# Optimization experiments

Measured on AMD Instinct MI355X. Metric: run time of the kernel, lower is better.

## Reference

```python
import jax, jax.numpy as jnp
import numpy as np

N = 50000
E = 1600000
IN_CH = 128
HID = 32
HEADS = 4
OUT_CH = 64
NEG_SLOPE = 0.2


def _seg_softmax(e, seg, n):
    # e: [E,H], seg: [E] destination indices -> per-destination softmax
    m = jax.ops.segment_max(e, seg, num_segments=n)          # [N,H]
    ex = jnp.exp(e - m[seg])
    s = jax.ops.segment_sum(ex, seg, num_segments=n)         # [N,H]
    return ex / (s[seg] + 1e-16)


def _gat_conv(x, edge_index, W, a_src, a_dst, b, concat):
    # x: [N,Fin]; W: [Fin, H*C]; a_src/a_dst: [H,C]; b: [H*C] or [C]
    H, C = a_src.shape
    n = x.shape[0]
    h = (x @ W).reshape(n, H, C)                              # [N,H,C]
    src, dst = edge_index[0], edge_index[1]
    as_ = jnp.einsum('nhc,hc->nh', h, a_src)                  # [N,H]
    ad_ = jnp.einsum('nhc,hc->nh', h, a_dst)
    e = jax.nn.leaky_relu(as_[src] + ad_[dst], NEG_SLOPE)     # [E,H]
    alpha = _seg_softmax(e, dst, n)                           # [E,H]
    msg = h[src] * alpha[:, :, None]                          # [E,H,C]
    out = jax.ops.segment_sum(msg, dst, num_segments=n)       # [N,H,C]
    out = out.reshape(n, H * C) if concat else out.mean(axis=1)
    return out + b, alpha


def _layer_norm(x, w, b, eps=1e-5):
    mu = x.mean(-1, keepdims=True)
    var = x.var(-1, keepdims=True)
    return (x - mu) * jax.lax.rsqrt(var + eps) * w + b


def setup_inputs() -> dict:
    key = jax.random.key(0)
    ks = jax.random.split(key, 20)
    g = lambda k, s: jax.random.normal(k, s, dtype=jnp.float32) * 0.05
    d = {
        'x': jax.random.normal(ks[0], (N, IN_CH), dtype=jnp.float32),
        'edge_index': jax.random.randint(ks[1], (2, E), 0, N, dtype=jnp.int64),
        # gat1: in=IN_CH, out=HID, heads, concat
        'W1': g(ks[2], (IN_CH, HEADS * HID)),
        'a_src1': g(ks[3], (HEADS, HID)),
        'a_dst1': g(ks[4], (HEADS, HID)),
        'b1': jnp.zeros((HEADS * HID,), jnp.float32),
        'ln1_w': jnp.ones((HEADS * HID,), jnp.float32),
        'ln1_b': jnp.zeros((HEADS * HID,), jnp.float32),
        'Wskip': g(ks[5], (IN_CH, HEADS * HID)),
        'bskip': jnp.zeros((HEADS * HID,), jnp.float32),
        # gat2: in=HEADS*HID, out=HID, concat
        'W2': g(ks[6], (HEADS * HID, HEADS * HID)),
        'a_src2': g(ks[7], (HEADS, HID)),
        'a_dst2': g(ks[8], (HEADS, HID)),
        'b2': jnp.zeros((HEADS * HID,), jnp.float32),
        'ln2_w': jnp.ones((HEADS * HID,), jnp.float32),
        'ln2_b': jnp.zeros((HEADS * HID,), jnp.float32),
        # gat3: in=HEADS*HID, out=OUT_CH, concat=False (mean over heads)
        'W3': g(ks[9], (HEADS * HID, HEADS * OUT_CH)),
        'a_src3': g(ks[10], (HEADS, OUT_CH)),
        'a_dst3': g(ks[11], (HEADS, OUT_CH)),
        'b3': jnp.zeros((OUT_CH,), jnp.float32),
    }
    return d


def reference(x, edge_index, W1, a_src1, a_dst1, b1, ln1_w, ln1_b,
              Wskip, bskip, W2, a_src2, a_dst2, b2, ln2_w, ln2_b,
              W3, a_src3, a_dst3, b3):
    x_skip = x
    h, alpha1 = _gat_conv(x, edge_index, W1, a_src1, a_dst1, b1, concat=True)
    h = jax.nn.elu(h)
    h = _layer_norm(h, ln1_w, ln1_b)
    h = h + (x_skip @ Wskip + bskip)
    h, alpha2 = _gat_conv(h, edge_index, W2, a_src2, a_dst2, b2, concat=True)
    h = jax.nn.elu(h)
    h = _layer_norm(h, ln2_w, ln2_b)
    out, alpha3 = _gat_conv(h, edge_index, W3, a_src3, a_dst3, b3, concat=False)
    return out, alpha1, alpha2, alpha3
```

## Files before the change

kernel.cpp:

```cpp
#include <hip/hip_runtime.h>

#define NN 50000
#define EE 1600000
#define SCAN_B 196
#define NB 196
#define CHUNK 2048
#define G1 782
#define L1 (NB * G1)
#define B1 599

typedef __attribute__((ext_vector_type(8))) short bf16x8;
typedef __attribute__((ext_vector_type(4))) float f32x4;
typedef __attribute__((ext_vector_type(2))) float f32x2;

#if __has_builtin(__builtin_elementwise_fma)
#define PKFMA(a, b, c) __builtin_elementwise_fma((a), (b), (c))
#else
#define PKFMA(a, b, c) ((a) * (b) + (c))
#endif

__device__ __forceinline__ float bfu(unsigned short u) { return __uint_as_float((unsigned)u << 16); }
__device__ __forceinline__ float bflo(unsigned u) { return __uint_as_float(u << 16); }
__device__ __forceinline__ float bfhi(unsigned u) { return __uint_as_float(u & 0xffff0000u); }
__device__ __forceinline__ f32x2 bfpk(unsigned u) {
    f32x2 r; r.x = bflo(u); r.y = bfhi(u); return r;
}
__device__ __forceinline__ unsigned short f2bf(float f) {
    unsigned u = __float_as_uint(f);
    u += 0x7fff + ((u >> 16) & 1);
    return (unsigned short)(u >> 16);
}
__device__ __forceinline__ unsigned pk2(float a, float b) {
    return (unsigned)f2bf(a) | ((unsigned)f2bf(b) << 16);
}
__device__ __forceinline__ float cvt_load(const void* p, int i, bool f32) {
    if (f32) return ((const float*)p)[i];
    return bfu(((const unsigned short*)p)[i]);
}

__global__ void detect_k(const void* ei_raw, const void* x_raw, int* flags) {
    __shared__ int s_i64, s_f32;
    const int t = threadIdx.x;
    if (t == 0) { s_i64 = 1; s_f32 = 0; }
    __syncthreads();
    const int* ei32 = (const int*)ei_raw;
    if (ei32[2 * t + 1] != 0) atomicAnd(&s_i64, 0);
    const unsigned short* xu = (const unsigned short*)x_raw;
    int found = 0;
    for (int j = 0; j < 32; j++) {
        unsigned short u = xu[t * 32 + j];
        if ((u & 0x7F80) == 0x7F80) found = 1;
    }
    if (found) atomicOr(&s_f32, 1);
    __syncthreads();
    if (t == 0) { flags[0] = s_i64; flags[1] = s_f32; }
}

__global__ __launch_bounds__(256) void hist1_k(const void* ei_raw, const int* flags,
                                               int2* __restrict__ edges, int* __restrict__ cnt)
{
    __shared__ int h[NB];
    const int t = threadIdx.x;
    const int i64 = __builtin_amdgcn_readfirstlane(flags[0]);
    if (t < NB) h[t] = 0;
    __syncthreads();
    const int beg = blockIdx.x * CHUNK;
    const int end = min(beg + CHUNK, EE);
    for (int e = beg + t; e < end; e += 256) {
        int2 v;
        if (i64) { const long long* p = (const long long*)ei_raw; v.x = (int)p[e]; v.y = (int)p[EE + e]; }
        else     { const int* p = (const int*)ei_raw;             v.x = p[e];      v.y = p[EE + e];      }
        edges[e] = v;
        atomicAdd(&h[v.y >> 8], 1);
    }
    __syncthreads();
    if (t < NB) cnt[(size_t)t * G1 + blockIdx.x] = h[t];
}

__global__ __launch_bounds__(256) void scanAg_k(int* __restrict__ cnt, int* __restrict__ bsum2) {
    __shared__ int ps[256];
    const int b = blockIdx.x, t = threadIdx.x;
    const int i = b * 256 + t;
    const int v = (i < L1) ? cnt[i] : 0;
    ps[t] = v;
    __syncthreads();
    for (int off = 1; off < 256; off <<= 1) {
        const int u = (t >= off) ? ps[t - off] : 0;
        __syncthreads();
        ps[t] += u;
        __syncthreads();
    }
    if (i < L1) cnt[i] = ps[t] - v;
    if (t == 255) bsum2[b] = ps[255];
}
__global__ void scanBg_k(int* bsum2) {
    __shared__ int ps[256];
    const int t = threadIdx.x;
    int vals[3];
    int s = 0;
    #pragma unroll
    for (int i = 0; i < 3; i++) {
        const int idx = t * 3 + i;
        vals[i] = (idx < B1) ? bsum2[idx] : 0;
        s += vals[i];
    }
    ps[t] = s;
    __syncthreads();
    for (int off = 1; off < 256; off <<= 1) {
        const int u = (t >= off) ? ps[t - off] : 0;
        __syncthreads();
        ps[t] += u;
        __syncthreads();
    }
    int run = t ? ps[t - 1] : 0;
    #pragma unroll
    for (int i = 0; i < 3; i++) {
        const int idx = t * 3 + i;
        if (idx < B1) bsum2[idx] = run;
        run += vals[i];
    }
}
__global__ __launch_bounds__(256) void scanCg_k(int* __restrict__ cnt, const int* __restrict__ bsum2,
                                                int* __restrict__ bstart) {
    const int i = blockIdx.x * 256 + threadIdx.x;
    if (i < L1) {
        const int r = cnt[i] + bsum2[blockIdx.x];
        cnt[i] = r;
        if (i % G1 == 0) bstart[i / G1] = r;
    }
    if (i == 0) bstart[NB] = EE;
}

__global__ __launch_bounds__(256) void scatter_k(const int2* __restrict__ edges,
                                                 const int* __restrict__ cnt,
                                                 int2* __restrict__ bedges)
{
    __shared__ int ofs[NB];
    const int t = threadIdx.x;
    if (t < NB) ofs[t] = cnt[(size_t)t * G1 + blockIdx.x];
    __syncthreads();
    const int beg = blockIdx.x * CHUNK;
    const int end = min(beg + CHUNK, EE);
    for (int e = beg + t; e < end; e += 256) {
        const int2 v = edges[e];
        const int p = atomicAdd(&ofs[v.y >> 8], 1);
        bedges[p] = v;
    }
}

__global__ __launch_bounds__(256) void hist_k(const int2* __restrict__ bedges,
                                              const int* __restrict__ bstart, int* __restrict__ deg)
{
    __shared__ int h[256];
    const int b = blockIdx.x, t = threadIdx.x;
    h[t] = 0;
    __syncthreads();
    const int lo = bstart[b], hi = bstart[b + 1];
    for (int i = lo + t; i < hi; i += 256)
        atomicAdd(&h[bedges[i].y & 255], 1);
    __syncthreads();
    const int d = b * 256 + t;
    if (d < NN) deg[d] = h[t];
}

__global__ __launch_bounds__(256) void scanA_k(const int* __restrict__ deg,
                                               int* __restrict__ roff, int* __restrict__ bsum) {
    __shared__ int ps[256];
    const int b = blockIdx.x, t = threadIdx.x;
    const int i = b * 256 + t;
    const int v = (i < NN) ? deg[i] : 0;
    ps[t] = v;
    __syncthreads();
    for (int off = 1; off < 256; off <<= 1) {
        const int u = (t >= off) ? ps[t - off] : 0;
        __syncthreads();
        ps[t] += u;
        __syncthreads();
    }
    if (i < NN) roff[i] = ps[t] - v;
    if (t == 255) bsum[b] = ps[255];
}
__global__ void scanB_k(int* bsum) {
    __shared__ int ps[256];
    const int t = threadIdx.x;
    const int v = (t < SCAN_B) ? bsum[t] : 0;
    ps[t] = v;
    __syncthreads();
    for (int off = 1; off < 256; off <<= 1) {
        const int u = (t >= off) ? ps[t - off] : 0;
        __syncthreads();
        ps[t] += u;
        __syncthreads();
    }
    if (t < SCAN_B) bsum[t] = ps[t] - v;
}
__global__ __launch_bounds__(256) void scanC_k(int* __restrict__ roff, const int* __restrict__ bsum) {
    const int b = blockIdx.x, t = threadIdx.x;
    const int i = b * 256 + t;
    if (i < NN) roff[i] += bsum[b];
}

__global__ __launch_bounds__(256) void place_k(const int2* __restrict__ bedges,
                                               const int* __restrict__ bstart, const int* __restrict__ roff,
                                               int* __restrict__ csrc)
{
    __shared__ int cur[256];
    const int b = blockIdx.x, t = threadIdx.x;
    const int d = b * 256 + t;
    cur[t] = (d < NN) ? roff[d] : 0;
    __syncthreads();
    const int lo = bstart[b], hi = bstart[b + 1];
    for (int i = lo + t; i < hi; i += 256) {
        const int2 v = bedges[i];
        const int p = atomicAdd(&cur[v.y & 255], 1);
        csrc[p] = v.x;
    }
}

__global__ __launch_bounds__(256) void cvt_all_k(
    const void* x, const void* W1, const void* Wskip, const void* W2, const void* W3,
    const void* as1, const void* ad1, const void* b1, const void* l1w, const void* l1b,
    const void* bsk, const void* as2, const void* ad2, const void* b2, const void* l2w,
    const void* l2b, const void* as3, const void* ad3, const void* b3,
    unsigned short* xb, unsigned short* Wt1, unsigned short* Wts, unsigned short* Wt2,
    unsigned short* Wt3, float* smalls, const int* flags)
{
    const bool f32 = __builtin_amdgcn_readfirstlane(flags[1]) != 0;
    const int gid = blockIdx.x * 256 + threadIdx.x;
    if (gid < NN * 128) { xb[gid] = f2bf(cvt_load(x, gid, f32)); return; }
    int g = gid - NN * 128;
    if (g < 16384) { Wt1[g] = f2bf(cvt_load(W1,    (g & 127) * 128 + (g >> 7), f32)); return; }
    g -= 16384;
    if (g < 16384) { Wts[g] = f2bf(cvt_load(Wskip, (g & 127) * 128 + (g >> 7), f32)); return; }
    g -= 16384;
    if (g < 16384) { Wt2[g] = f2bf(cvt_load(W2,    (g & 127) * 128 + (g >> 7), f32)); return; }
    g -= 16384;
    if (g < 32768) { Wt3[g] = f2bf(cvt_load(W3,    (g & 127) * 256 + (g >> 7), f32)); return; }
    g -= 32768;
    if (g >= 2432) return;
    const void* src; int off;
    if      (g < 128)  { src = as1; off = g;        }
    else if (g < 256)  { src = ad1; off = g - 128;  }
    else if (g < 384)  { src = b1;  off = g - 256;  }
    else if (g < 512)  { src = l1w; off = g - 384;  }
    else if (g < 640)  { src = l1b; off = g - 512;  }
    else if (g < 768)  { src = bsk; off = g - 640;  }
    else if (g < 896)  { src = as2; off = g - 768;  }
    else if (g < 1024) { src = ad2; off = g - 896;  }
    else if (g < 1152) { src = b2;  off = g - 1024; }
    else if (g < 1280) { src = l2w; off = g - 1152; }
    else if (g < 1408) { src = l2b; off = g - 1280; }
    else if (g < 1664) { src = as3; off = g - 1408; }
    else if (g < 1920) { src = ad3; off = g - 1664; }
    else               { src = b3;  off = g - 1920; }
    smalls[g] = cvt_load(src, off, f32);
}

__global__ void prep_v_k(const unsigned short* __restrict__ Wt3, const float* __restrict__ as3,
                         const float* __restrict__ ad3, float* __restrict__ vsrc, float* __restrict__ vdst)
{
    const int t = blockIdx.x * 256 + threadIdx.x;
    if (t >= 512) return;
    const int h = t >> 7, k = t & 127;
    float ss = 0.f, dd = 0.f;
    for (int c = 0; c < 64; c++) {
        const float w = bfu(Wt3[(size_t)(h * 64 + c) * 128 + k]);
        ss = fmaf(w, as3[h * 64 + c], ss);
        dd = fmaf(w, ad3[h * 64 + c], dd);
    }
    vsrc[t] = ss; vdst[t] = dd;
}

template<int FOUT, bool DOTS>
__global__ __launch_bounds__(256) void mfma_mm_k(
    const unsigned short* __restrict__ Xb, const unsigned short* __restrict__ Wt,
    unsigned short* __restrict__ Hb,
    const float* __restrict__ asrc, const float* __restrict__ adst,
    float* __restrict__ as_, float* __restrict__ dpk)
{
    constexpr int NT = FOUT / 16;
    const int tile = blockIdx.x * 4 + (threadIdx.x >> 6);
    if (tile >= 3125) return;
    const int l = threadIdx.x & 63;
    const int lr = l & 15, lq = l >> 4;
    const int m0 = tile * 16;
    f32x4 acc[NT];
    #pragma unroll
    for (int nt = 0; nt < NT; nt++) { acc[nt][0]=0.f; acc[nt][1]=0.f; acc[nt][2]=0.f; acc[nt][3]=0.f; }
    #pragma unroll
    for (int kb = 0; kb < 4; kb++) {
        const bf16x8 a = *(const bf16x8*)(Xb + (size_t)(m0 + lr) * 128 + kb * 32 + lq * 8);
        #pragma unroll
        for (int nt = 0; nt < NT; nt++) {
            const bf16x8 b = *(const bf16x8*)(Wt + (size_t)(nt * 16 + lr) * 128 + kb * 32 + lq * 8);
            acc[nt] = __builtin_amdgcn_mfma_f32_16x16x32_bf16(a, b, acc[nt], 0, 0, 0);
        }
    }
    #pragma unroll
    for (int nt = 0; nt < NT; nt++)
        #pragma unroll
        for (int r = 0; r < 4; r++)
            Hb[(size_t)(m0 + lq * 4 + r) * FOUT + nt * 16 + lr] = f2bf(acc[nt][r]);
    if (DOTS) {
        #pragma unroll
        for (int hd = 0; hd < 4; hd++) {
            const float a0 = asrc[hd * 32 + lr], a1 = asrc[hd * 32 + 16 + lr];
            const float d0 = adst[hd * 32 + lr], d1 = adst[hd * 32 + 16 + lr];
            #pragma unroll
            for (int r = 0; r < 4; r++) {
                float ps = acc[2 * hd][r] * a0 + acc[2 * hd + 1][r] * a1;
                float pd = acc[2 * hd][r] * d0 + acc[2 * hd + 1][r] * d1;
                #pragma unroll
                for (int m = 8; m; m >>= 1) { ps += __shfl_xor(ps, m); pd += __shfl_xor(pd, m); }
                if (lr == 0) {
                    const int node = m0 + lq * 4 + r;
                    as_[(size_t)node * 4 + hd] = ps;
                    dpk[(size_t)node * 8 + hd] = pd;
                }
            }
        }
    }
}

__global__ __launch_bounds__(256) void mm12_k(
    const unsigned short* __restrict__ Xb, const unsigned short* __restrict__ Wt1,
    unsigned short* __restrict__ Hb, unsigned short* __restrict__ Sb,
    const float* __restrict__ asrc, const float* __restrict__ adst,
    float* __restrict__ as_, float* __restrict__ dpk)
{
    const int tile = blockIdx.x * 4 + (threadIdx.x >> 6);
    if (tile >= 3125) return;
    const int l = threadIdx.x & 63;
    const int lr = l & 15, lq = l >> 4;
    const int m0 = tile * 16;
    f32x4 acc[16];
    #pragma unroll
    for (int nt = 0; nt < 16; nt++) { acc[nt][0]=0.f; acc[nt][1]=0.f; acc[nt][2]=0.f; acc[nt][3]=0.f; }
    #pragma unroll
    for (int kb = 0; kb < 4; kb++) {
        const bf16x8 a = *(const bf16x8*)(Xb + (size_t)(m0 + lr) * 128 + kb * 32 + lq * 8);
        #pragma unroll
        for (int nt = 0; nt < 16; nt++) {
            const bf16x8 b = *(const bf16x8*)(Wt1 + (size_t)(nt * 16 + lr) * 128 + kb * 32 + lq * 8);
            acc[nt] = __builtin_amdgcn_mfma_f32_16x16x32_bf16(a, b, acc[nt], 0, 0, 0);
        }
    }
    #pragma unroll
    for (int nt = 0; nt < 8; nt++)
        #pragma unroll
        for (int r = 0; r < 4; r++)
            Hb[(size_t)(m0 + lq * 4 + r) * 128 + nt * 16 + lr] = f2bf(acc[nt][r]);
    #pragma unroll
    for (int nt = 8; nt < 16; nt++)
        #pragma unroll
        for (int r = 0; r < 4; r++)
            Sb[(size_t)(m0 + lq * 4 + r) * 128 + (nt - 8) * 16 + lr] = f2bf(acc[nt][r]);
    #pragma unroll
    for (int hd = 0; hd < 4; hd++) {
        const float a0 = asrc[hd * 32 + lr], a1 = asrc[hd * 32 + 16 + lr];
        const float d0 = adst[hd * 32 + lr], d1 = adst[hd * 32 + 16 + lr];
        #pragma unroll
        for (int r = 0; r < 4; r++) {
            float ps = acc[2 * hd][r] * a0 + acc[2 * hd + 1][r] * a1;
            float pd = acc[2 * hd][r] * d0 + acc[2 * hd + 1][r] * d1;
            #pragma unroll
            for (int m = 8; m; m >>= 1) { ps += __shfl_xor(ps, m); pd += __shfl_xor(pd, m); }
            if (lr == 0) {
                const int node = m0 + lq * 4 + r;
                as_[(size_t)node * 4 + hd] = ps;
                dpk[(size_t)node * 8 + hd] = pd;
            }
        }
    }
}

__device__ __forceinline__ float4 edge_w(float4 as4, float4 ad4) {
    float4 e4;
    e4.x = as4.x + ad4.x; e4.y = as4.y + ad4.y; e4.z = as4.z + ad4.z; e4.w = as4.w + ad4.w;
    e4.x = e4.x >= 0.f ? e4.x : 0.2f * e4.x;
    e4.y = e4.y >= 0.f ? e4.y : 0.2f * e4.y;
    e4.z = e4.z >= 0.f ? e4.z : 0.2f * e4.z;
    e4.w = e4.w >= 0.f ? e4.w : 0.2f * e4.w;
    float4 w4;
    w4.x = __expf(e4.x); w4.y = __expf(e4.y); w4.z = __expf(e4.z); w4.w = __expf(e4.w);
    return w4;
}

template<bool HAS_SKIP, bool DOTS3>
__global__ __launch_bounds__(256) void fagg12_k(
    const int* __restrict__ roff, const int* __restrict__ deg,
    const int* __restrict__ csrc, const float* __restrict__ as_, float* __restrict__ dpk,
    const unsigned short* __restrict__ Hb,
    const float* __restrict__ b, const float* __restrict__ lnw, const float* __restrict__ lnb,
    const unsigned short* __restrict__ skipb, const float* __restrict__ bskip,
    unsigned short* __restrict__ xoutb,
    const float* __restrict__ vsrc, const float* __restrict__ vdst,
    float* __restrict__ as3o, float* __restrict__ dpk3o)
{
    __shared__ float lws[4][512];
    const int warp = threadIdx.x >> 6;
    const int lane = threadIdx.x & 63;
    const int half = lane >> 5;
    const int l32  = lane & 31;
    const int node = blockIdx.x * 8 + warp * 2 + half;
    const int q = l32 & 15, g = l32 >> 4;
    const int h = q >> 2;
    float* lw = lws[warp] + half * 256;
    const int ro = roff[node], dg = deg[node];
    const float4 ad4 = *(const float4*)(dpk + (size_t)node * 8);

    float4 sv = make_float4(0.f, 0.f, 0.f, 0.f);
    f32x2 acc2[4];
    #pragma unroll
    for (int i = 0; i < 4; i++) { acc2[i].x = 0.f; acc2[i].y = 0.f; }

    for (int j0 = 0; j0 < dg; j0 += 32) {
        const int jn = min(32, dg - j0);
        int src = 0;
        float4 w4 = make_float4(0.f, 0.f, 0.f, 0.f);
        if (l32 < jn) {
            src = csrc[ro + j0 + l32];
            const float4 as4 = *(const float4*)(as_ + (size_t)src * 4);
            w4 = edge_w(as4, ad4);
            sv.x += w4.x; sv.y += w4.y; sv.z += w4.z; sv.w += w4.w;
        }
        const float sf = __int_as_float(src);
        *(float4*)(lw + l32 * 8)     = make_float4(w4.x, sf, w4.y, sf);
        *(float4*)(lw + l32 * 8 + 4) = make_float4(w4.z, sf, w4.w, sf);
        const int jq = (jn + 1) >> 1;
        #pragma unroll 2
        for (int j = 0; j < jq; j++) {
            const int e = 2 * j + g;
            const float2 rd = *(const float2*)(lw + e * 8 + h * 2);
            f32x2 ww; ww.x = rd.x; ww.y = rd.x;
            const unsigned soff = (__float_as_uint(rd.y) << 8) + (unsigned)(q << 4);
            const uint4 hv = *(const uint4*)((const char*)Hb + soff);
            acc2[0] = PKFMA(ww, bfpk(hv.x), acc2[0]);
            acc2[1] = PKFMA(ww, bfpk(hv.y), acc2[1]);
            acc2[2] = PKFMA(ww, bfpk(hv.z), acc2[2]);
            acc2[3] = PKFMA(ww, bfpk(hv.w), acc2[3]);
        }
    }

    #pragma unroll
    for (int i = 0; i < 4; i++) {
        acc2[i].x += __shfl_xor(acc2[i].x, 16);
        acc2[i].y += __shfl_xor(acc2[i].y, 16);
    }
    #pragma unroll
    for (int m = 16; m; m >>= 1) {
        sv.x += __shfl_xor(sv.x, m); sv.y += __shfl_xor(sv.y, m);
        sv.z += __shfl_xor(sv.z, m); sv.w += __shfl_xor(sv.w, m);
    }
    float4 rs;
    rs.x = 1.f / (sv.x + 1e-16f); rs.y = 1.f / (sv.y + 1e-16f);
    rs.z = 1.f / (sv.z + 1e-16f); rs.w = 1.f / (sv.w + 1e-16f);
    if (l32 == 0) *(float4*)(dpk + (size_t)node * 8 + 4) = rs;
    const float rsh = (h == 0) ? rs.x : (h == 1) ? rs.y : (h == 2) ? rs.z : rs.w;

    const float4 b0 = *(const float4*)(b + q * 8);
    const float4 b1 = *(const float4*)(b + q * 8 + 4);
    float v[8];
    v[0] = acc2[0].x * rsh + b0.x; v[1] = acc2[0].y * rsh + b0.y;
    v[2] = acc2[1].x * rsh + b0.z; v[3] = acc2[1].y * rsh + b0.w;
    v[4] = acc2[2].x * rsh + b1.x; v[5] = acc2[2].y * rsh + b1.y;
    v[6] = acc2[3].x * rsh + b1.z; v[7] = acc2[3].y * rsh + b1.w;
    float s1 = 0.f, s2 = 0.f;
    #pragma unroll
    for (int i = 0; i < 8; i++) {
        v[i] = v[i] > 0.f ? v[i] : (__expf(v[i]) - 1.f);
        s1 += v[i]; s2 += v[i] * v[i];
    }
    #pragma unroll
    for (int m = 8; m; m >>= 1) { s1 += __shfl_xor(s1, m); s2 += __shfl_xor(s2, m); }
    const float mu   = s1 * (1.f / 128.f);
    const float var  = s2 * (1.f / 128.f) - mu * mu;
    const float rstd = rsqrtf(var + 1e-5f);
    const float4 w0 = *(const float4*)(lnw + q * 8);
    const float4 w1 = *(const float4*)(lnw + q * 8 + 4);
    const float4 o0 = *(const float4*)(lnb + q * 8);
    const float4 o1 = *(const float4*)(lnb + q * 8 + 4);
    float y[8];
    y[0] = (v[0] - mu) * rstd * w0.x + o0.x; y[1] = (v[1] - mu) * rstd * w0.y + o0.y;
    y[2] = (v[2] - mu) * rstd * w0.z + o0.z; y[3] = (v[3] - mu) * rstd * w0.w + o0.w;
    y[4] = (v[4] - mu) * rstd * w1.x + o1.x; y[5] = (v[5] - mu) * rstd * w1.y + o1.y;
    y[6] = (v[6] - mu) * rstd * w1.z + o1.z; y[7] = (v[7] - mu) * rstd * w1.w + o1.w;
    if (HAS_SKIP) {
        const uint4 sk = *(const uint4*)(skipb + (size_t)node * 128 + q * 8);
        const float4 k0 = *(const float4*)(bskip + q * 8);
        const float4 k1 = *(const float4*)(bskip + q * 8 + 4);
        y[0] += bflo(sk.x) + k0.x; y[1] += bfhi(sk.x) + k0.y;
        y[2] += bflo(sk.y) + k0.z; y[3] += bfhi(sk.y) + k0.w;
        y[4] += bflo(sk.z) + k1.x; y[5] += bfhi(sk.z) + k1.y;
        y[6] += bflo(sk.w) + k1.z; y[7] += bfhi(sk.w) + k1.w;
    }
    if (g == 0) {
        uint4 pk;
        pk.x = pk2(y[0], y[1]); pk.y = pk2(y[2], y[3]);
        pk.z = pk2(y[4], y[5]); pk.w = pk2(y[6], y[7]);
        *(uint4*)(xoutb + (size_t)node * 128 + q * 8) = pk;
    }
    if (DOTS3) {
        #pragma unroll
        for (int hd = 0; hd < 4; hd++) {
            const float4 vs0 = *(const float4*)(vsrc + hd * 128 + q * 8);
            const float4 vs1 = *(const float4*)(vsrc + hd * 128 + q * 8 + 4);
            const float4 vd0 = *(const float4*)(vdst + hd * 128 + q * 8);
            const float4 vd1 = *(const float4*)(vdst + hd * 128 + q * 8 + 4);
            float ss = y[0] * vs0.x + y[1] * vs0.y + y[2] * vs0.z + y[3] * vs0.w
                     + y[4] * vs1.x + y[5] * vs1.y + y[6] * vs1.z + y[7] * vs1.w;
            float dd = y[0] * vd0.x + y[1] * vd0.y + y[2] * vd0.z + y[3] * vd0.w
                     + y[4] * vd1.x + y[5] * vd1.y + y[6] * vd1.z + y[7] * vd1.w;
            #pragma unroll
            for (int m = 8; m; m >>= 1) { ss += __shfl_xor(ss, m); dd += __shfl_xor(dd, m); }
            if (l32 == 0) {
                as3o[(size_t)node * 4 + hd] = ss;
                dpk3o[(size_t)node * 8 + hd] = dd;
            }
        }
    }
}

__global__ __launch_bounds__(256) void fagg3_k(
    const int* __restrict__ roff, const int* __restrict__ deg,
    const int* __restrict__ csrc, const float* __restrict__ as_, float* __restrict__ dpk,
    const unsigned short* __restrict__ Xb,
    unsigned short* __restrict__ gout)
{
    __shared__ float lws[4][256];
    __shared__ int lss[4][64];
    const int warp = threadIdx.x >> 6;
    const int lane = threadIdx.x & 63;
    const int half = lane >> 5;
    const int l32  = lane & 31;
    const int node = blockIdx.x * 8 + warp * 2 + half;
    float* lw = lws[warp] + half * 128;
    int*   ls = lss[warp] + half * 32;
    const int ro = roff[node], dg = deg[node];
    const float4 ad4 = *(const float4*)(dpk + (size_t)node * 8);

    float4 sv = make_float4(0.f, 0.f, 0.f, 0.f);
    f32x2 acc2[4][2];
    #pragma unroll
    for (int hh = 0; hh < 4; hh++)
        #pragma unroll
        for (int i = 0; i < 2; i++) { acc2[hh][i].x = 0.f; acc2[hh][i].y = 0.f; }

    for (int j0 = 0; j0 < dg; j0 += 32) {
        const int jn = min(32, dg - j0);
        int src = 0;
        float4 w4 = make_float4(0.f, 0.f, 0.f, 0.f);
        if (l32 < jn) {
            src = csrc[ro + j0 + l32];
            const float4 as4 = *(const float4*)(as_ + (size_t)src * 4);
            w4 = edge_w(as4, ad4);
            sv.x += w4.x; sv.y += w4.y; sv.z += w4.z; sv.w += w4.w;
        }
        *(float4*)(lw + l32 * 4) = w4;
        ls[l32] = src;
        for (int j = 0; j < jn; j++) {
            const float4 w = *(const float4*)(lw + j * 4);
            const int s_ = ls[j];
            const unsigned soff = ((unsigned)s_ << 8) + (unsigned)(l32 << 3);
            const uint2 hv = *(const uint2*)((const char*)Xb + soff);
            const f32x2 x01 = bfpk(hv.x), x23 = bfpk(hv.y);
            f32x2 w0; w0.x = w.x; w0.y = w.x;
            f32x2 w1; w1.x = w.y; w1.y = w.y;
            f32x2 w2; w2.x = w.z; w2.y = w.z;
            f32x2 w3; w3.x = w.w; w3.y = w.w;
            acc2[0][0] = PKFMA(w0, x01, acc2[0][0]); acc2[0][1] = PKFMA(w0, x23, acc2[0][1]);
            acc2[1][0] = PKFMA(w1, x01, acc2[1][0]); acc2[1][1] = PKFMA(w1, x23, acc2[1][1]);
            acc2[2][0] = PKFMA(w2, x01, acc2[2][0]); acc2[2][1] = PKFMA(w2, x23, acc2[2][1]);
            acc2[3][0] = PKFMA(w3, x01, acc2[3][0]); acc2[3][1] = PKFMA(w3, x23, acc2[3][1]);
        }
    }

    #pragma unroll
    for (int m = 16; m; m >>= 1) {
        sv.x += __shfl_xor(sv.x, m); sv.y += __shfl_xor(sv.y, m);
        sv.z += __shfl_xor(sv.z, m); sv.w += __shfl_xor(sv.w, m);
    }
    float4 rs;
    rs.x = 1.f / (sv.x + 1e-16f); rs.y = 1.f / (sv.y + 1e-16f);
    rs.z = 1.f / (sv.z + 1e-16f); rs.w = 1.f / (sv.w + 1e-16f);
    if (l32 == 0) *(float4*)(dpk + (size_t)node * 8 + 4) = rs;

    unsigned short* gr = gout + (size_t)node * 512 + 4 * l32;
    uint2 p0, p1, p2, p3;
    p0.x = pk2(acc2[0][0].x * rs.x, acc2[0][0].y * rs.x);
    p0.y = pk2(acc2[0][1].x * rs.x, acc2[0][1].y * rs.x);
    p1.x = pk2(acc2[1][0].x * rs.y, acc2[1][0].y * rs.y);
    p1.y = pk2(acc2[1][1].x * rs.y, acc2[1][1].y * rs.y);
    p2.x = pk2(acc2[2][0].x * rs.z, acc2[2][0].y * rs.z);
    p2.y = pk2(acc2[2][1].x * rs.z, acc2[2][1].y * rs.z);
    p3.x = pk2(acc2[3][0].x * rs.w, acc2[3][0].y * rs.w);
    p3.y = pk2(acc2[3][1].x * rs.w, acc2[3][1].y * rs.w);
    *(uint2*)(gr)       = p0;
    *(uint2*)(gr + 128) = p1;
    *(uint2*)(gr + 256) = p2;
    *(uint2*)(gr + 384) = p3;
}

__global__ __launch_bounds__(256) void alpha_l_k(
    const int2* __restrict__ edges, const float* __restrict__ as_,
    const float* __restrict__ dpk, float* __restrict__ al)
{
    const int e = blockIdx.x * 256 + threadIdx.x;
    const int2 v = edges[e];
    const float4 as4 = *(const float4*)(as_ + (size_t)v.x * 4);
    const float4 ad4 = *(const float4*)(dpk + (size_t)v.y * 8);
    const float4 r   = *(const float4*)(dpk + (size_t)v.y * 8 + 4);
    const float4 w = edge_w(as4, ad4);
    float4 a; a.x = w.x * r.x; a.y = w.y * r.y; a.z = w.z * r.z; a.w = w.w * r.w;
    *(float4*)(al + (size_t)e * 4) = a;
}

__global__ __launch_bounds__(256) void proj3_k(
    const unsigned short* __restrict__ Gb, const unsigned short* __restrict__ Wt3,
    const float* __restrict__ b3, float* __restrict__ out)
{
    const int tile = blockIdx.x * 4 + (threadIdx.x >> 6);
    if (tile >= 3125) return;
    const int l = threadIdx.x & 63;
    const int lr = l & 15, lq = l >> 4;
    const int m0 = tile * 16;
    f32x4 acc[4];
    #pragma unroll
    for (int nt = 0; nt < 4; nt++) { acc[nt][0]=0.f; acc[nt][1]=0.f; acc[nt][2]=0.f; acc[nt][3]=0.f; }
    #pragma unroll
    for (int kb = 0; kb < 16; kb++) {
        const int h = kb >> 2;
        const int kk = (kb & 3) * 32 + lq * 8;
        const bf16x8 a = *(const bf16x8*)(Gb + (size_t)(m0 + lr) * 512 + kb * 32 + lq * 8);
        #pragma unroll
        for (int nt = 0; nt < 4; nt++) {
            const int c = nt * 16 + lr;
            const bf16x8 b = *(const bf16x8*)(Wt3 + (size_t)(h * 64 + c) * 128 + kk);
            acc[nt] = __builtin_amdgcn_mfma_f32_16x16x32_bf16(a, b, acc[nt], 0, 0, 0);
        }
    }
    #pragma unroll
    for (int nt = 0; nt < 4; nt++)
        #pragma unroll
        for (int r = 0; r < 4; r++) {
            const int col = nt * 16 + lr;
            out[(size_t)(m0 + lq * 4 + r) * 64 + col] = 0.25f * acc[nt][r] + b3[col];
        }
}

extern "C" void kernel_launch(void* const* d_in, const int* in_sizes, int n_in,
                              void* d_out, int out_size, void* d_ws, size_t ws_size,
                              hipStream_t stream)
{
    char* ws = (char*)d_ws;
    unsigned short* g_bf    = (unsigned short*)(ws);
    int2*           bedges  = (int2*)(ws);
    int*            csrc    = (int*)(ws + 51200000);
    unsigned short* x_bf    = (unsigned short*)(ws + 57600000);
    unsigned short* xcur_bf = (unsigned short*)(ws + 70400000);
    unsigned short* skip_bf = (unsigned short*)(ws + 83200000);
    unsigned short* Hbuf    = (unsigned short*)(ws + 96000000);
    int2*  edges  = (int2*)(ws + 108800000);
    float* as1b   = (float*)(ws + 121600000);
    float* as2b   = as1b + 200000;
    float* as3b   = as1b + 400000;
    float* dpk1   = as1b + 600000;
    float* dpk2   = as1b + 1000000;
    float* dpk3   = as1b + 1400000;
    int*   roff   = (int*)(ws + 128800000);
    int*   deg    = (int*)(ws + 129000000);
    int*   bsum   = (int*)(ws + 129200000);
    int*   flags  = (int*)(ws + 129402048);
    unsigned short* Wt1 = (unsigned short*)(ws + 129500000);
    unsigned short* Wts = Wt1 + 16384;
    unsigned short* Wt2 = Wts + 16384;
    unsigned short* Wt3 = Wt2 + 16384;
    float* smalls = (float*)(ws + 129700000);
    float* vsrc   = (float*)(ws + 129720000);
    float* vdst   = (float*)(ws + 129730000);
    int*   cnt    = (int*)(ws + 130000000);
    int*   bsum2  = (int*)(ws + 130700000);
    int*   bstart = (int*)(ws + 130710000);

    float* as1c = smalls;          float* ad1c = smalls + 128;
    float* b1c  = smalls + 256;    float* l1wc = smalls + 384;
    float* l1bc = smalls + 512;    float* bskc = smalls + 640;
    float* as2c = smalls + 768;    float* ad2c = smalls + 896;
    float* b2c  = smalls + 1024;   float* l2wc = smalls + 1152;
    float* l2bc = smalls + 1280;   float* as3c = smalls + 1408;
    float* ad3c = smalls + 1664;   float* b3c  = smalls + 1920;

    float* out = (float*)d_out;
    float* al1 = out + (size_t)NN * 64;
    float* al2 = al1 + (size_t)EE * 4;
    float* al3 = al2 + (size_t)EE * 4;

    detect_k<<<1, 256, 0, stream>>>(d_in[1], d_in[0], flags);
    hist1_k<<<G1, 256, 0, stream>>>(d_in[1], flags, edges, cnt);
    cvt_all_k<<<25330, 256, 0, stream>>>(
        d_in[0], d_in[2], d_in[8], d_in[10], d_in[16],
        d_in[3], d_in[4], d_in[5], d_in[6], d_in[7],
        d_in[9], d_in[11], d_in[12], d_in[13], d_in[14], d_in[15],
        d_in[17], d_in[18], d_in[19],
        x_bf, Wt1, Wts, Wt2, Wt3, smalls, flags);
    scanAg_k<<<B1, 256, 0, stream>>>(cnt, bsum2);
    scanBg_k<<<1, 256, 0, stream>>>(bsum2);
    scanCg_k<<<B1, 256, 0, stream>>>(cnt, bsum2, bstart);
    scatter_k<<<G1, 256, 0, stream>>>(edges, cnt, bedges);
    hist_k<<<NB, 256, 0, stream>>>(bedges, bstart, deg);
    scanA_k<<<SCAN_B, 256, 0, stream>>>(deg, roff, bsum);
    scanB_k<<<1, 256, 0, stream>>>(bsum);
    scanC_k<<<SCAN_B, 256, 0, stream>>>(roff, bsum);
    place_k<<<NB, 256, 0, stream>>>(bedges, bstart, roff, csrc);
    prep_v_k<<<2, 256, 0, stream>>>(Wt3, as3c, ad3c, vsrc, vdst);

    mm12_k<<<782, 256, 0, stream>>>(x_bf, Wt1, Hbuf, skip_bf, as1c, ad1c, as1b, dpk1);
    fagg12_k<true, false><<<6250, 256, 0, stream>>>(roff, deg, csrc, as1b, dpk1, Hbuf,
                                                    b1c, l1wc, l1bc, skip_bf, bskc, xcur_bf,
                                                    nullptr, nullptr, nullptr, nullptr);

    mfma_mm_k<128, true><<<782, 256, 0, stream>>>(xcur_bf, Wt2, Hbuf, as2c, ad2c, as2b, dpk2);
    fagg12_k<false, true><<<6250, 256, 0, stream>>>(roff, deg, csrc, as2b, dpk2, Hbuf,
                                                    b2c, l2wc, l2bc, nullptr, nullptr, xcur_bf,
                                                    vsrc, vdst, as3b, dpk3);

    fagg3_k<<<6250, 256, 0, stream>>>(roff, deg, csrc, as3b, dpk3, xcur_bf, g_bf);
    proj3_k<<<782, 256, 0, stream>>>(g_bf, Wt3, b3c, out);

    alpha_l_k<<<6250, 256, 0, stream>>>(edges, as1b, dpk1, al1);
    alpha_l_k<<<6250, 256, 0, stream>>>(edges, as2b, dpk2, al2);
    alpha_l_k<<<6250, 256, 0, stream>>>(edges, as3b, dpk3, al3);
}
```

Before: 570.2 us.

## Fold degree histogram into hist1 with global atomics; unroll gather loops

The separate hist_k kernel is removed. Per-node degree is now counted with global atomicAdd inside hist1_k, after a memset of deg. This drops one launch and one pass over the bucketed edges, at the cost of 1.6M global atomics that may contend. The layer-1/2 aggregation inner loop unroll rises from 2 to 4. The layer-3 aggregation loop is manually unrolled by 4 so more independent gather loads are in flight at once.

```diff
diff --git a/kernel.cpp b/kernel.cpp
--- a/kernel.cpp
+++ b/kernel.cpp
@@ -57,7 +57,8 @@
 }
 
 __global__ __launch_bounds__(256) void hist1_k(const void* ei_raw, const int* flags,
-                                               int2* __restrict__ edges, int* __restrict__ cnt)
+                                               int2* __restrict__ edges, int* __restrict__ cnt,
+                                               int* __restrict__ deg)
 {
     __shared__ int h[NB];
     const int t = threadIdx.x;
@@ -72,6 +73,7 @@
         else     { const int* p = (const int*)ei_raw;             v.x = p[e];      v.y = p[EE + e];      }
         edges[e] = v;
         atomicAdd(&h[v.y >> 8], 1);
+        atomicAdd(&deg[v.y], 1);
     }
     __syncthreads();
     if (t < NB) cnt[(size_t)t * G1 + blockIdx.x] = h[t];
@@ -146,21 +148,6 @@
         const int p = atomicAdd(&ofs[v.y >> 8], 1);
         bedges[p] = v;
     }
-}
-
-__global__ __launch_bounds__(256) void hist_k(const int2* __restrict__ bedges,
-                                              const int* __restrict__ bstart, int* __restrict__ deg)
-{
-    __shared__ int h[256];
-    const int b = blockIdx.x, t = threadIdx.x;
-    h[t] = 0;
-    __syncthreads();
-    const int lo = bstart[b], hi = bstart[b + 1];
-    for (int i = lo + t; i < hi; i += 256)
-        atomicAdd(&h[bedges[i].y & 255], 1);
-    __syncthreads();
-    const int d = b * 256 + t;
-    if (d < NN) deg[d] = h[t];
 }
 
 __global__ __launch_bounds__(256) void scanA_k(const int* __restrict__ deg,
@@ -428,7 +415,7 @@
         *(float4*)(lw + l32 * 8)     = make_float4(w4.x, sf, w4.y, sf);
         *(float4*)(lw + l32 * 8 + 4) = make_float4(w4.z, sf, w4.w, sf);
         const int jq = (jn + 1) >> 1;
-        #pragma unroll 2
+        #pragma unroll 4
         for (int j = 0; j < jq; j++) {
             const int e = 2 * j + g;
             const float2 rd = *(const float2*)(lw + e * 8 + h * 2);
@@ -546,6 +533,21 @@
         #pragma unroll
         for (int i = 0; i < 2; i++) { acc2[hh][i].x = 0.f; acc2[hh][i].y = 0.f; }
 
+    const unsigned myoff = (unsigned)(l32 << 3);
+
+    #define F3_FMA(W4, HV)                                                              \
+        {                                                                               \
+            const f32x2 x01 = bfpk((HV).x), x23 = bfpk((HV).y);                         \
+            f32x2 w0; w0.x = (W4).x; w0.y = (W4).x;                                     \
+            f32x2 w1; w1.x = (W4).y; w1.y = (W4).y;                                     \
+            f32x2 w2; w2.x = (W4).z; w2.y = (W4).z;                                     \
+            f32x2 w3; w3.x = (W4).w; w3.y = (W4).w;                                     \
+            acc2[0][0] = PKFMA(w0, x01, acc2[0][0]); acc2[0][1] = PKFMA(w0, x23, acc2[0][1]); \
+            acc2[1][0] = PKFMA(w1, x01, acc2[1][0]); acc2[1][1] = PKFMA(w1, x23, acc2[1][1]); \
+            acc2[2][0] = PKFMA(w2, x01, acc2[2][0]); acc2[2][1] = PKFMA(w2, x23, acc2[2][1]); \
+            acc2[3][0] = PKFMA(w3, x01, acc2[3][0]); acc2[3][1] = PKFMA(w3, x23, acc2[3][1]); \
+        }
+
     for (int j0 = 0; j0 < dg; j0 += 32) {
         const int jn = min(32, dg - j0);
         int src = 0;
@@ -558,22 +560,39 @@
         }
         *(float4*)(lw + l32 * 4) = w4;
         ls[l32] = src;
-        for (int j = 0; j < jn; j++) {
-            const float4 w = *(const float4*)(lw + j * 4);
-            const int s_ = ls[j];
-            const unsigned soff = ((unsigned)s_ << 8) + (unsigned)(l32 << 3);
-            const uint2 hv = *(const uint2*)((const char*)Xb + soff);
-            const f32x2 x01 = bfpk(hv.x), x23 = bfpk(hv.y);
-            f32x2 w0; w0.x = w.x; w0.y = w.x;
-            f32x2 w1; w1.x = w.y; w1.y = w.y;
-            f32x2 w2; w2.x = w.z; w2.y = w.z;
-            f32x2 w3; w3.x = w.w; w3.y = w.w;
-            acc2[0][0] = PKFMA(w0, x01, acc2[0][0]); acc2[0][1] = PKFMA(w0, x23, acc2[0][1]);
-            acc2[1][0] = PKFMA(w1, x01, acc2[1][0]); acc2[1][1] = PKFMA(w1, x23, acc2[1][1]);
-            acc2[2][0] = PKFMA(w2, x01, acc2[2][0]); acc2[2][1] = PKFMA(w2, x23, acc2[2][1]);
-            acc2[3][0] = PKFMA(w3, x01, acc2[3][0]); acc2[3][1] = PKFMA(w3, x23, acc2[3][1]);
-        }
-    }
+        int j = 0;
+        for (; j + 4 <= jn; j += 4) {
+            const float4 wa = *(const float4*)(lw + j * 4);
+            const float4 wb = *(const float4*)(lw + j * 4 + 4);
+            const float4 wc = *(const float4*)(lw + j * 4 + 8);
+            const float4 wd = *(const float4*)(lw + j * 4 + 12);
+            const int sa = ls[j], sb = ls[j + 1], sc = ls[j + 2], sd = ls[j + 3];
+            const uint2 ha = *(const uint2*)((const char*)Xb + (((unsigned)sa) << 8) + myoff);
+            const uint2 hb = *(const uint2*)((const char*)Xb + (((unsigned)sb) << 8) + myoff);
+            const uint2 hc = *(const uint2*)((const char*)Xb + (((unsigned)sc) << 8) + myoff);
+            const uint2 hd = *(const uint2*)((const char*)Xb + (((unsigned)sd) << 8) + myoff);
+            F3_FMA(wa, ha)
+            F3_FMA(wb, hb)
+            F3_FMA(wc, hc)
+            F3_FMA(wd, hd)
+        }
+        for (; j + 2 <= jn; j += 2) {
+            const float4 wa = *(const float4*)(lw + j * 4);
+            const float4 wb = *(const float4*)(lw + j * 4 + 4);
+            const int sa = ls[j], sb = ls[j + 1];
+            const uint2 ha = *(const uint2*)((const char*)Xb + (((unsigned)sa) << 8) + myoff);
+            const uint2 hb = *(const uint2*)((const char*)Xb + (((unsigned)sb) << 8) + myoff);
+            F3_FMA(wa, ha)
+            F3_FMA(wb, hb)
+        }
+        if (j < jn) {
+            const float4 wa = *(const float4*)(lw + j * 4);
+            const int sa = ls[j];
+            const uint2 ha = *(const uint2*)((const char*)Xb + (((unsigned)sa) << 8) + myoff);
+            F3_FMA(wa, ha)
+        }
+    }
+    #undef F3_FMA
 
     #pragma unroll
     for (int m = 16; m; m >>= 1) {
@@ -696,7 +715,8 @@
     float* al3 = al2 + (size_t)EE * 4;
 
     detect_k<<<1, 256, 0, stream>>>(d_in[1], d_in[0], flags);
-    hist1_k<<<G1, 256, 0, stream>>>(d_in[1], flags, edges, cnt);
+    hipMemsetAsync(deg, 0, NN * sizeof(int), stream);
+    hist1_k<<<G1, 256, 0, stream>>>(d_in[1], flags, edges, cnt, deg);
     cvt_all_k<<<25330, 256, 0, stream>>>(
         d_in[0], d_in[2], d_in[8], d_in[10], d_in[16],
         d_in[3], d_in[4], d_in[5], d_in[6], d_in[7],
@@ -707,7 +727,6 @@
     scanBg_k<<<1, 256, 0, stream>>>(bsum2);
     scanCg_k<<<B1, 256, 0, stream>>>(cnt, bsum2, bstart);
     scatter_k<<<G1, 256, 0, stream>>>(edges, cnt, bedges);
-    hist_k<<<NB, 256, 0, stream>>>(bedges, bstart, deg);
     scanA_k<<<SCAN_B, 256, 0, stream>>>(deg, roff, bsum);
     scanB_k<<<1, 256, 0, stream>>>(bsum);
     scanC_k<<<SCAN_B, 256, 0, stream>>>(roff, bsum);
```

Result: slower. 623.1 us (+9.3%).
